# Optimization experiments

Hardware: AMD Instinct MI355X
Metric: run time of the kernel (lower is better)

Reference implementation:

```python
import jax, jax.numpy as jnp
import numpy as np

N_EXPERTS = 8
TOP_K = 2
D_MODEL = 1024
D_INNER = 4096
BATCH = 8
SEQ = 2048


def setup_inputs() -> dict:
    key = jax.random.key(0)
    k_x, k_g, k_e = jax.random.split(key, 3)
    sequences = jax.random.normal(k_x, (BATCH, SEQ, D_MODEL), dtype=jnp.float32)
    # gating Linear(d_model -> n_experts)
    gating_w = jax.random.normal(k_g, (N_EXPERTS, D_MODEL), dtype=jnp.float32) * (1.0 / np.sqrt(D_MODEL))
    gating_b = jnp.zeros((N_EXPERTS,), dtype=jnp.float32)
    # expert Linear(d_model -> d_inner), xavier_uniform
    xav = float(np.sqrt(6.0 / (D_MODEL + D_INNER)))
    expert_w = jax.random.uniform(k_e, (N_EXPERTS, D_INNER, D_MODEL), dtype=jnp.float32, minval=-xav, maxval=xav)
    expert_b = jnp.zeros((N_EXPERTS, D_INNER), dtype=jnp.float32)
    return {"sequences": sequences, "gating_w": gating_w, "gating_b": gating_b,
            "expert_w": expert_w, "expert_b": expert_b}


def reference(sequences, gating_w, gating_b, expert_w, expert_b):
    N, P, D = sequences.shape
    x = sequences.reshape(N * P, D)                                  # [T, D]
    gating_scores = jax.nn.softmax(x @ gating_w.T + gating_b, axis=-1)  # [T, E]
    _, top_k_indices = jax.lax.top_k(gating_scores, TOP_K)          # [T, K]
    # mask[t, e] = expert e is among token t's top-k (indices are distinct)
    mask = (top_k_indices[:, :, None] == jnp.arange(N_EXPERTS)[None, None, :]).any(axis=1)  # [T, E]
    maskf = mask.astype(x.dtype)
    out = jnp.zeros((N * P, D_INNER), dtype=x.dtype)
    for e in range(N_EXPERTS):  # small fixed expert count
        out = out + maskf[:, e:e + 1] * (x @ expert_w[e].T + expert_b[e])
    out = out / TOP_K
    # training-mode auxiliary: per-expert variance of gating scores (unbiased, like torch.var)
    gating_variances = jnp.var(gating_scores, axis=0, ddof=1)        # [E]
    return out.reshape(N, P, D_INNER), gating_variances
```

## Files before the change

### kernel.cpp

```cpp
#include <hip/hip_runtime.h>

#define T_TOKENS 16384
#define DM 1024
#define DI 4096
#define NE 8
#define PAIRS 64
#define CAP 16384

typedef float f32x4 __attribute__((ext_vector_type(4)));
typedef __bf16 bf16x8 __attribute__((ext_vector_type(8)));

__device__ inline unsigned short f2b(float f) {
  union { float f; unsigned u; } v; v.f = f;
  unsigned r = v.u + 0x7FFFu + ((v.u >> 16) & 1u);
  return (unsigned short)(r >> 16);
}

__global__ __launch_bounds__(256) void k_gating(
    const float* __restrict__ x, const float* __restrict__ gw, const float* __restrict__ gb,
    unsigned short* __restrict__ x16, float* __restrict__ scores,
    int* __restrict__ cnt, int* __restrict__ ptok)
{
  int wid  = (blockIdx.x * 256 + threadIdx.x) >> 6;
  int lane = threadIdx.x & 63;
  if (wid >= T_TOKENS) return;
  const float* xr = x + (size_t)wid * DM;

  double acc[NE];
  #pragma unroll
  for (int e = 0; e < NE; e++) acc[e] = 0.0;

  #pragma unroll
  for (int u = 0; u < 4; u++) {
    int off = u * 256 + lane * 4;
    float4 xv = *(const float4*)(xr + off);
    ushort4 pk; pk.x = f2b(xv.x); pk.y = f2b(xv.y); pk.z = f2b(xv.z); pk.w = f2b(xv.w);
    *(ushort4*)(x16 + (size_t)wid * DM + off) = pk;
    #pragma unroll
    for (int e = 0; e < NE; e++) {
      float4 wv = *(const float4*)(gw + e * DM + off);
      acc[e] += (double)xv.x * wv.x + (double)xv.y * wv.y
              + (double)xv.z * wv.z + (double)xv.w * wv.w;
    }
  }
  #pragma unroll
  for (int e = 0; e < NE; e++) {
    double v = acc[e];
    #pragma unroll
    for (int s = 32; s > 0; s >>= 1) v += __shfl_xor(v, s, 64);
    acc[e] = v + (double)gb[e];
  }
  if (lane == 0) {
    double m = acc[0];
    for (int e = 1; e < NE; e++) if (acc[e] > m) m = acc[e];
    double ex[NE], sum = 0.0;
    for (int e = 0; e < NE; e++) { ex[e] = exp(acc[e] - m); sum += ex[e]; }
    double inv = 1.0 / sum;
    for (int e = 0; e < NE; e++) scores[(size_t)wid * NE + e] = (float)(ex[e] * inv);
    int e1 = 0; double b1 = acc[0];
    for (int e = 1; e < NE; e++) if (acc[e] > b1) { b1 = acc[e]; e1 = e; }
    int e2 = -1; double b2 = -1e300;
    for (int e = 0; e < NE; e++) if (e != e1 && acc[e] > b2) { b2 = acc[e]; e2 = e; }
    int lo = e1 < e2 ? e1 : e2, hi = e1 < e2 ? e2 : e1;
    int p = lo * 8 + hi;
    int pos = atomicAdd(&cnt[p], 1);
    ptok[p * CAP + pos] = wid;
  }
}

__global__ __launch_bounds__(256) void k_wconv(const float* __restrict__ w, unsigned short* __restrict__ w16) {
  size_t i = ((size_t)blockIdx.x * 256 + threadIdx.x) * 8;
  float4 a = *(const float4*)(w + i);
  float4 b = *(const float4*)(w + i + 4);
  ushort4 pa, pb;
  pa.x = f2b(a.x); pa.y = f2b(a.y); pa.z = f2b(a.z); pa.w = f2b(a.w);
  pb.x = f2b(b.x); pb.y = f2b(b.y); pb.z = f2b(b.z); pb.w = f2b(b.w);
  *(ushort4*)(w16 + i) = pa;
  *(ushort4*)(w16 + i + 4) = pb;
}

__global__ void k_sched(const int* __restrict__ cnt, int* __restrict__ tiles, int* __restrict__ ntiles) {
  int p = threadIdx.x;
  int c = cnt[p];
  int nt = (c + 127) >> 7;
  int inc = nt;
  #pragma unroll
  for (int s = 1; s < 64; s <<= 1) {
    int v = __shfl_up(inc, s, 64);
    if (p >= s) inc += v;
  }
  int excl = inc - nt;
  for (int i = 0; i < nt; i++) { tiles[2 * (excl + i)] = p; tiles[2 * (excl + i) + 1] = i * 128; }
  if (p == 63) *ntiles = inc;
}

__global__ __launch_bounds__(256) void k_gemm(
    const unsigned short* __restrict__ x16, const unsigned short* __restrict__ w16,
    const float* __restrict__ eb, const int* __restrict__ cnt,
    const int* __restrict__ ptok, const int* __restrict__ tiles, const int* __restrict__ ntiles,
    float* __restrict__ out)
{
  __shared__ unsigned short As[128 * 64];
  __shared__ unsigned short Bs[2][128 * 64];

  int tileIdx = blockIdx.y;
  if (tileIdx >= *ntiles) return;
  int p    = tiles[2 * tileIdx];
  int row0 = tiles[2 * tileIdx + 1];
  int e1 = p >> 3, e2 = p & 7;
  int c  = cnt[p];
  int nTile = blockIdx.x;
  int tid  = threadIdx.x;
  int lane = tid & 63;
  int wid  = tid >> 6;
  int waveM = wid >> 1, waveN = wid & 1;

  int rlim = c - row0 - waveM * 64;

  int tok[4];
  #pragma unroll
  for (int i = 0; i < 4; i++) {
    int rg = row0 + (tid >> 3) + i * 32;
    if (rg > c - 1) rg = c - 1;
    tok[i] = ptok[p * CAP + rg];
  }

  f32x4 acc[4][4];
  #pragma unroll
  for (int i = 0; i < 4; i++)
    #pragma unroll
    for (int j = 0; j < 4; j++) acc[i][j] = {0.f, 0.f, 0.f, 0.f};

  const unsigned short* bb1 = w16 + ((size_t)e1 * DI + (size_t)nTile * 128) * DM;
  const unsigned short* bb2 = w16 + ((size_t)e2 * DI + (size_t)nTile * 128) * DM;

  for (int k0 = 0; k0 < DM; k0 += 64) {
    #pragma unroll
    for (int i = 0; i < 4; i++) {
      int r  = (tid >> 3) + i * 32;
      int cS = tid & 7;
      int kg = ((cS ^ (r & 7)) * 8);
      __builtin_amdgcn_global_load_lds(
          (const __attribute__((address_space(1))) void*)(x16 + (size_t)tok[i] * DM + k0 + kg),
          (__attribute__((address_space(3))) void*)(&As[r * 64 + cS * 8]), 16, 0, 0);
      __builtin_amdgcn_global_load_lds(
          (const __attribute__((address_space(1))) void*)(bb1 + (size_t)r * DM + k0 + kg),
          (__attribute__((address_space(3))) void*)(&Bs[0][r * 64 + cS * 8]), 16, 0, 0);
      __builtin_amdgcn_global_load_lds(
          (const __attribute__((address_space(1))) void*)(bb2 + (size_t)r * DM + k0 + kg),
          (__attribute__((address_space(3))) void*)(&Bs[1][r * 64 + cS * 8]), 16, 0, 0);
    }
    __syncthreads();
    #pragma unroll
    for (int kk = 0; kk < 2; kk++) {
      int q  = lane >> 4;
      int m  = lane & 15;
      int jg = kk * 4 + q;
      bf16x8 af[4], bf0[4], bf1[4];
      #pragma unroll
      for (int mi = 0; mi < 4; mi++) {
        if (mi * 16 < rlim) {
          int R = waveM * 64 + mi * 16 + m;
          af[mi] = *(const bf16x8*)&As[R * 64 + ((jg ^ (R & 7)) * 8)];
        }
      }
      #pragma unroll
      for (int ni = 0; ni < 4; ni++) {
        int R = waveN * 64 + ni * 16 + m;
        int o = R * 64 + ((jg ^ (R & 7)) * 8);
        bf0[ni] = *(const bf16x8*)&Bs[0][o];
        bf1[ni] = *(const bf16x8*)&Bs[1][o];
      }
      #pragma unroll
      for (int mi = 0; mi < 4; mi++) {
        if (mi * 16 < rlim) {
          #pragma unroll
          for (int ni = 0; ni < 4; ni++) {
            acc[mi][ni] = __builtin_amdgcn_mfma_f32_16x16x32_bf16(af[mi], bf0[ni], acc[mi][ni], 0, 0, 0);
            acc[mi][ni] = __builtin_amdgcn_mfma_f32_16x16x32_bf16(af[mi], bf1[ni], acc[mi][ni], 0, 0, 0);
          }
        }
      }
    }
    __syncthreads();
  }

  int colbase = nTile * 128 + waveN * 64;
  float bsum[4];
  #pragma unroll
  for (int ni = 0; ni < 4; ni++) {
    int col = colbase + ni * 16 + (lane & 15);
    bsum[ni] = 0.5f * (eb[e1 * DI + col] + eb[e2 * DI + col]);
  }
  #pragma unroll
  for (int mi = 0; mi < 4; mi++) {
    #pragma unroll
    for (int r2 = 0; r2 < 4; r2++) {
      int row = waveM * 64 + mi * 16 + (lane >> 4) * 4 + r2;
      int rg = row0 + row;
      if (rg < c) {
        int t = ptok[p * CAP + rg];
        float* orow = out + (size_t)t * DI + colbase;
        #pragma unroll
        for (int ni = 0; ni < 4; ni++)
          orow[ni * 16 + (lane & 15)] = 0.5f * acc[mi][ni][r2] + bsum[ni];
      }
    }
  }
}

__global__ __launch_bounds__(256) void k_var(const float* __restrict__ scores, float* __restrict__ vout) {
  int e = blockIdx.x, tid = threadIdx.x;
  double s = 0.0, s2 = 0.0;
  for (int t = tid; t < T_TOKENS; t += 256) {
    double v = (double)scores[(size_t)t * NE + e];
    s += v; s2 += v * v;
  }
  __shared__ double ls[256], ls2[256];
  ls[tid] = s; ls2[tid] = s2; __syncthreads();
  for (int st = 128; st > 0; st >>= 1) {
    if (tid < st) { ls[tid] += ls[tid + st]; ls2[tid] += ls2[tid + st]; }
    __syncthreads();
  }
  if (tid == 0) {
    double mean = ls[0] / (double)T_TOKENS;
    vout[e] = (float)((ls2[0] - ls[0] * mean) / (double)(T_TOKENS - 1));
  }
}

extern "C" void kernel_launch(void* const* d_in, const int* in_sizes, int n_in,
                              void* d_out, int out_size, void* d_ws, size_t ws_size,
                              hipStream_t stream)
{
  const float* x  = (const float*)d_in[0];
  const float* gw = (const float*)d_in[1];
  const float* gb = (const float*)d_in[2];
  const float* ew = (const float*)d_in[3];
  const float* eb = (const float*)d_in[4];
  float* out = (float*)d_out;

  char* ws = (char*)d_ws;
  unsigned short* x16 = (unsigned short*)ws;
  unsigned short* w16 = (unsigned short*)(ws + 33554432);
  float* scores       = (float*)(ws + 100663296);
  int*   ptok         = (int*)(ws + 101187584);
  int*   cnt          = (int*)(ws + 105381888);
  int*   ntiles       = (int*)(ws + 105382144);
  int*   tiles        = (int*)(ws + 105382160);

  hipMemsetAsync(cnt, 0, PAIRS * sizeof(int), stream);
  k_gating<<<dim3(4096), dim3(256), 0, stream>>>(x, gw, gb, x16, scores, cnt, ptok);
  k_wconv <<<dim3(16384), dim3(256), 0, stream>>>(ew, w16);
  k_sched <<<dim3(1), dim3(64), 0, stream>>>(cnt, tiles, ntiles);
  k_gemm  <<<dim3(32, 192), dim3(256), 0, stream>>>(x16, w16, eb, cnt, ptok, tiles, ntiles, out);
  k_var   <<<dim3(8), dim3(256), 0, stream>>>(scores, out + 67108864);
}
```

Baseline: 770.8 us.

## Double-buffer LDS tiles with K=32 stages to overlap loads with MFMA

Changes the GEMM main loop from single-buffered K=64 tiles with two barriers per step to double-buffered K=32 tiles. The next stage's global-to-LDS loads are issued before computing on the current buffer, leaving one barrier per step. LDS use stays the same, the swizzle is adapted to 32-wide rows, and launch bounds request 3 blocks per CU. The costs are twice as many iterations and barriers, and more register pressure from the occupancy hint.

```diff
diff --git a/kernel.cpp b/kernel.cpp
--- a/kernel.cpp
+++ b/kernel.cpp
@@ -94,14 +94,14 @@
   if (p == 63) *ntiles = inc;
 }
 
-__global__ __launch_bounds__(256) void k_gemm(
+__global__ __launch_bounds__(256, 3) void k_gemm(
     const unsigned short* __restrict__ x16, const unsigned short* __restrict__ w16,
     const float* __restrict__ eb, const int* __restrict__ cnt,
     const int* __restrict__ ptok, const int* __restrict__ tiles, const int* __restrict__ ntiles,
     float* __restrict__ out)
 {
-  __shared__ unsigned short As[128 * 64];
-  __shared__ unsigned short Bs[2][128 * 64];
+  __shared__ unsigned short As[2][128 * 32];
+  __shared__ unsigned short Bs[2][2][128 * 32];
 
   int tileIdx = blockIdx.y;
   if (tileIdx >= *ntiles) return;
@@ -117,10 +117,10 @@
 
   int rlim = c - row0 - waveM * 64;
 
-  int tok[4];
-  #pragma unroll
-  for (int i = 0; i < 4; i++) {
-    int rg = row0 + (tid >> 3) + i * 32;
+  int tok[2];
+  #pragma unroll
+  for (int i = 0; i < 2; i++) {
+    int rg = row0 + (tid >> 2) + i * 64;
     if (rg > c - 1) rg = c - 1;
     tok[i] = ptok[p * CAP + rg];
   }
@@ -134,56 +134,66 @@
   const unsigned short* bb1 = w16 + ((size_t)e1 * DI + (size_t)nTile * 128) * DM;
   const unsigned short* bb2 = w16 + ((size_t)e2 * DI + (size_t)nTile * 128) * DM;
 
-  for (int k0 = 0; k0 < DM; k0 += 64) {
-    #pragma unroll
-    for (int i = 0; i < 4; i++) {
-      int r  = (tid >> 3) + i * 32;
-      int cS = tid & 7;
-      int kg = ((cS ^ (r & 7)) * 8);
-      __builtin_amdgcn_global_load_lds(
-          (const __attribute__((address_space(1))) void*)(x16 + (size_t)tok[i] * DM + k0 + kg),
-          (__attribute__((address_space(3))) void*)(&As[r * 64 + cS * 8]), 16, 0, 0);
-      __builtin_amdgcn_global_load_lds(
-          (const __attribute__((address_space(1))) void*)(bb1 + (size_t)r * DM + k0 + kg),
-          (__attribute__((address_space(3))) void*)(&Bs[0][r * 64 + cS * 8]), 16, 0, 0);
-      __builtin_amdgcn_global_load_lds(
-          (const __attribute__((address_space(1))) void*)(bb2 + (size_t)r * DM + k0 + kg),
-          (__attribute__((address_space(3))) void*)(&Bs[1][r * 64 + cS * 8]), 16, 0, 0);
-    }
-    __syncthreads();
-    #pragma unroll
-    for (int kk = 0; kk < 2; kk++) {
-      int q  = lane >> 4;
-      int m  = lane & 15;
-      int jg = kk * 4 + q;
-      bf16x8 af[4], bf0[4], bf1[4];
-      #pragma unroll
-      for (int mi = 0; mi < 4; mi++) {
-        if (mi * 16 < rlim) {
-          int R = waveM * 64 + mi * 16 + m;
-          af[mi] = *(const bf16x8*)&As[R * 64 + ((jg ^ (R & 7)) * 8)];
+#define STAGE(buf, k0s)                                                                           \
+  {                                                                                               \
+    _Pragma("unroll")                                                                             \
+    for (int i = 0; i < 2; i++) {                                                                 \
+      int r  = (tid >> 2) + i * 64;                                                               \
+      int cS = tid & 3;                                                                           \
+      int kg = ((cS ^ ((r >> 1) & 3)) * 8);               \
+      __builtin_amdgcn_global_load_lds(                                                           \
+          (const __attribute__((address_space(1))) void*)(x16 + (size_t)tok[i] * DM + (k0s) + kg),\
+          (__attribute__((address_space(3))) void*)(&As[buf][r * 32 + cS * 8]), 16, 0, 0);        \
+      __builtin_amdgcn_global_load_lds(                                                           \
+          (const __attribute__((address_space(1))) void*)(bb1 + (size_t)r * DM + (k0s) + kg),     \
+          (__attribute__((address_space(3))) void*)(&Bs[buf][0][r * 32 + cS * 8]), 16, 0, 0);     \
+      __builtin_amdgcn_global_load_lds(                                                           \
+          (const __attribute__((address_space(1))) void*)(bb2 + (size_t)r * DM + (k0s) + kg),     \
+          (__attribute__((address_space(3))) void*)(&Bs[buf][1][r * 32 + cS * 8]), 16, 0, 0);     \
+    }                                                                                             \
+  }
+
+  int cur = 0;
+  STAGE(0, 0);
+
+  #pragma unroll 2
+  for (int k0 = 0; k0 < DM; k0 += 32) {
+    asm volatile("s_waitcnt vmcnt(0)" ::: "memory");
+    __builtin_amdgcn_s_barrier();
+    __builtin_amdgcn_sched_barrier(0);
+
+    if (k0 + 32 < DM) { STAGE(cur ^ 1, k0 + 32); }
+
+    int q = lane >> 4;
+    int m = lane & 15;
+    bf16x8 af[4], bf0[4], bf1[4];
+    #pragma unroll
+    for (int mi = 0; mi < 4; mi++) {
+      if (mi * 16 < rlim) {
+        int R = waveM * 64 + mi * 16 + m;
+        af[mi] = *(const bf16x8*)&As[cur][R * 32 + ((q ^ ((R >> 1) & 3)) * 8)];
+      }
+    }
+    #pragma unroll
+    for (int ni = 0; ni < 4; ni++) {
+      int R = waveN * 64 + ni * 16 + m;
+      int o = R * 32 + ((q ^ ((R >> 1) & 3)) * 8);
+      bf0[ni] = *(const bf16x8*)&Bs[cur][0][o];
+      bf1[ni] = *(const bf16x8*)&Bs[cur][1][o];
+    }
+    #pragma unroll
+    for (int mi = 0; mi < 4; mi++) {
+      if (mi * 16 < rlim) {
+        #pragma unroll
+        for (int ni = 0; ni < 4; ni++) {
+          acc[mi][ni] = __builtin_amdgcn_mfma_f32_16x16x32_bf16(af[mi], bf0[ni], acc[mi][ni], 0, 0, 0);
+          acc[mi][ni] = __builtin_amdgcn_mfma_f32_16x16x32_bf16(af[mi], bf1[ni], acc[mi][ni], 0, 0, 0);
         }
       }
-      #pragma unroll
-      for (int ni = 0; ni < 4; ni++) {
-        int R = waveN * 64 + ni * 16 + m;
-        int o = R * 64 + ((jg ^ (R & 7)) * 8);
-        bf0[ni] = *(const bf16x8*)&Bs[0][o];
-        bf1[ni] = *(const bf16x8*)&Bs[1][o];
-      }
-      #pragma unroll
-      for (int mi = 0; mi < 4; mi++) {
-        if (mi * 16 < rlim) {
-          #pragma unroll
-          for (int ni = 0; ni < 4; ni++) {
-            acc[mi][ni] = __builtin_amdgcn_mfma_f32_16x16x32_bf16(af[mi], bf0[ni], acc[mi][ni], 0, 0, 0);
-            acc[mi][ni] = __builtin_amdgcn_mfma_f32_16x16x32_bf16(af[mi], bf1[ni], acc[mi][ni], 0, 0, 0);
-          }
-        }
-      }
-    }
-    __syncthreads();
-  }
+    }
+    cur ^= 1;
+  }
+#undef STAGE
 
   int colbase = nTile * 128 + waveN * 64;
   float bsum[4];
```

Result: slower. 790.8 us (+2.6%).

## Precombine expert-pair weights so each token tile runs a single GEMM

Applied to the files above, without the earlier changes.

Adds a kernel that builds averaged bf16 weight matrices for all 28 expert pairs, (W_lo+W_hi)/2. The grouped GEMM can then multiply each token tile by one pair matrix instead of accumulating two expert GEMMs, which halves the MFMA work and the B-operand traffic. The cost is writing 28 bf16 weight matrices (about 235 MB) per call instead of 8. Rounding the average to bf16 also changes numerics slightly. A fallback keeps the old dual-expert path when the workspace is too small, and the new GEMM uses a single B buffer with a launch-bounds occupancy hint.

```diff
diff --git a/kernel.cpp b/kernel.cpp
--- a/kernel.cpp
+++ b/kernel.cpp
@@ -5,6 +5,7 @@
 #define DI 4096
 #define NE 8
 #define PAIRS 64
+#define NPAIRC 28
 #define CAP 16384
 
 typedef float f32x4 __attribute__((ext_vector_type(4)));
@@ -79,6 +80,27 @@
   *(ushort4*)(w16 + i + 4) = pb;
 }
 
+__global__ __launch_bounds__(256) void k_wpair(const float* __restrict__ w, unsigned short* __restrict__ wp) {
+  size_t i = ((size_t)blockIdx.x * 256 + threadIdx.x) * 4;
+  float4 v[NE];
+  #pragma unroll
+  for (int e = 0; e < NE; e++) v[e] = *(const float4*)(w + (size_t)e * (DI * (size_t)DM) + i);
+  int idx = 0;
+  #pragma unroll
+  for (int lo = 0; lo < NE; lo++) {
+    #pragma unroll
+    for (int hi = lo + 1; hi < NE; hi++) {
+      ushort4 pk;
+      pk.x = f2b(0.5f * (v[lo].x + v[hi].x));
+      pk.y = f2b(0.5f * (v[lo].y + v[hi].y));
+      pk.z = f2b(0.5f * (v[lo].z + v[hi].z));
+      pk.w = f2b(0.5f * (v[lo].w + v[hi].w));
+      *(ushort4*)(wp + (size_t)idx * (DI * (size_t)DM) + i) = pk;
+      idx++;
+    }
+  }
+}
+
 __global__ void k_sched(const int* __restrict__ cnt, int* __restrict__ tiles, int* __restrict__ ntiles) {
   int p = threadIdx.x;
   int c = cnt[p];
@@ -94,7 +116,115 @@
   if (p == 63) *ntiles = inc;
 }
 
-__global__ __launch_bounds__(256) void k_gemm(
+__global__ __launch_bounds__(256, 5) void k_gemm_pair(
+    const unsigned short* __restrict__ x16, const unsigned short* __restrict__ wp,
+    const float* __restrict__ eb, const int* __restrict__ cnt,
+    const int* __restrict__ ptok, const int* __restrict__ tiles, const int* __restrict__ ntiles,
+    float* __restrict__ out)
+{
+  __shared__ unsigned short As[128 * 64];
+  __shared__ unsigned short Bs[128 * 64];
+
+  int tileIdx = blockIdx.y;
+  if (tileIdx >= *ntiles) return;
+  int p    = tiles[2 * tileIdx];
+  int row0 = tiles[2 * tileIdx + 1];
+  int e1 = p >> 3, e2 = p & 7;
+  int pidx = e1 * 7 - ((e1 * (e1 - 1)) >> 1) + (e2 - e1 - 1);
+  int c  = cnt[p];
+  int nTile = blockIdx.x;
+  int tid  = threadIdx.x;
+  int lane = tid & 63;
+  int wid  = tid >> 6;
+  int waveM = wid >> 1, waveN = wid & 1;
+
+  int rlim = c - row0 - waveM * 64;
+
+  int tok[4];
+  #pragma unroll
+  for (int i = 0; i < 4; i++) {
+    int rg = row0 + (tid >> 3) + i * 32;
+    if (rg > c - 1) rg = c - 1;
+    tok[i] = ptok[p * CAP + rg];
+  }
+
+  f32x4 acc[4][4];
+  #pragma unroll
+  for (int i = 0; i < 4; i++)
+    #pragma unroll
+    for (int j = 0; j < 4; j++) acc[i][j] = {0.f, 0.f, 0.f, 0.f};
+
+  const unsigned short* bb = wp + ((size_t)pidx * DI + (size_t)nTile * 128) * DM;
+
+  for (int k0 = 0; k0 < DM; k0 += 64) {
+    #pragma unroll
+    for (int i = 0; i < 4; i++) {
+      int r  = (tid >> 3) + i * 32;
+      int cS = tid & 7;
+      int kg = ((cS ^ (r & 7)) * 8);
+      __builtin_amdgcn_global_load_lds(
+          (const __attribute__((address_space(1))) void*)(x16 + (size_t)tok[i] * DM + k0 + kg),
+          (__attribute__((address_space(3))) void*)(&As[r * 64 + cS * 8]), 16, 0, 0);
+      __builtin_amdgcn_global_load_lds(
+          (const __attribute__((address_space(1))) void*)(bb + (size_t)r * DM + k0 + kg),
+          (__attribute__((address_space(3))) void*)(&Bs[r * 64 + cS * 8]), 16, 0, 0);
+    }
+    __syncthreads();
+    #pragma unroll
+    for (int kk = 0; kk < 2; kk++) {
+      int q  = lane >> 4;
+      int m  = lane & 15;
+      int jg = kk * 4 + q;
+      bf16x8 af[4], bf[4];
+      #pragma unroll
+      for (int mi = 0; mi < 4; mi++) {
+        if (mi * 16 < rlim) {
+          int R = waveM * 64 + mi * 16 + m;
+          af[mi] = *(const bf16x8*)&As[R * 64 + ((jg ^ (R & 7)) * 8)];
+        }
+      }
+      #pragma unroll
+      for (int ni = 0; ni < 4; ni++) {
+        int R = waveN * 64 + ni * 16 + m;
+        bf[ni] = *(const bf16x8*)&Bs[R * 64 + ((jg ^ (R & 7)) * 8)];
+      }
+      #pragma unroll
+      for (int mi = 0; mi < 4; mi++) {
+        if (mi * 16 < rlim) {
+          #pragma unroll
+          for (int ni = 0; ni < 4; ni++)
+            acc[mi][ni] = __builtin_amdgcn_mfma_f32_16x16x32_bf16(af[mi], bf[ni], acc[mi][ni], 0, 0, 0);
+        }
+      }
+    }
+    __syncthreads();
+  }
+
+  int colbase = nTile * 128 + waveN * 64;
+  float bsum[4];
+  #pragma unroll
+  for (int ni = 0; ni < 4; ni++) {
+    int col = colbase + ni * 16 + (lane & 15);
+    bsum[ni] = 0.5f * (eb[e1 * DI + col] + eb[e2 * DI + col]);
+  }
+  #pragma unroll
+  for (int mi = 0; mi < 4; mi++) {
+    #pragma unroll
+    for (int r2 = 0; r2 < 4; r2++) {
+      int row = waveM * 64 + mi * 16 + (lane >> 4) * 4 + r2;
+      int rg = row0 + row;
+      if (rg < c) {
+        int t = ptok[p * CAP + rg];
+        float* orow = out + (size_t)t * DI + colbase;
+        #pragma unroll
+        for (int ni = 0; ni < 4; ni++)
+          orow[ni * 16 + (lane & 15)] = acc[mi][ni][r2] + bsum[ni];
+      }
+    }
+  }
+}
+
+__global__ __launch_bounds__(256) void k_gemm_dual(
     const unsigned short* __restrict__ x16, const unsigned short* __restrict__ w16,
     const float* __restrict__ eb, const int* __restrict__ cnt,
     const int* __restrict__ ptok, const int* __restrict__ tiles, const int* __restrict__ ntiles,
@@ -114,7 +244,6 @@
   int lane = tid & 63;
   int wid  = tid >> 6;
   int waveM = wid >> 1, waveN = wid & 1;
-
   int rlim = c - row0 - waveM * 64;
 
   int tok[4];
@@ -238,20 +367,45 @@
   const float* ew = (const float*)d_in[3];
   const float* eb = (const float*)d_in[4];
   float* out = (float*)d_out;
-
   char* ws = (char*)d_ws;
-  unsigned short* x16 = (unsigned short*)ws;
-  unsigned short* w16 = (unsigned short*)(ws + 33554432);
-  float* scores       = (float*)(ws + 100663296);
-  int*   ptok         = (int*)(ws + 101187584);
-  int*   cnt          = (int*)(ws + 105381888);
-  int*   ntiles       = (int*)(ws + 105382144);
-  int*   tiles        = (int*)(ws + 105382160);
-
-  hipMemsetAsync(cnt, 0, PAIRS * sizeof(int), stream);
-  k_gating<<<dim3(4096), dim3(256), 0, stream>>>(x, gw, gb, x16, scores, cnt, ptok);
-  k_wconv <<<dim3(16384), dim3(256), 0, stream>>>(ew, w16);
-  k_sched <<<dim3(1), dim3(64), 0, stream>>>(cnt, tiles, ntiles);
-  k_gemm  <<<dim3(32, 192), dim3(256), 0, stream>>>(x16, w16, eb, cnt, ptok, tiles, ntiles, out);
-  k_var   <<<dim3(8), dim3(256), 0, stream>>>(scores, out + 67108864);
-}
+
+  const size_t OFF_WPAIR  = 33554432ull;
+  const size_t OFF_SCORES = OFF_WPAIR + (size_t)NPAIRC * DI * DM * 2;
+  const size_t OFF_PTOK   = OFF_SCORES + 524288ull;
+  const size_t OFF_CNT    = OFF_PTOK + 4194304ull;
+  const size_t OFF_NT     = OFF_CNT + 256ull;
+  const size_t OFF_TILES  = OFF_NT + 16ull;
+  const size_t NEED_PAIR  = OFF_TILES + 1536ull;
+
+  if (ws_size >= NEED_PAIR) {
+    unsigned short* x16 = (unsigned short*)ws;
+    unsigned short* wp  = (unsigned short*)(ws + OFF_WPAIR);
+    float* scores       = (float*)(ws + OFF_SCORES);
+    int*   ptok         = (int*)(ws + OFF_PTOK);
+    int*   cnt          = (int*)(ws + OFF_CNT);
+    int*   ntiles       = (int*)(ws + OFF_NT);
+    int*   tiles        = (int*)(ws + OFF_TILES);
+
+    hipMemsetAsync(cnt, 0, PAIRS * sizeof(int), stream);
+    k_gating<<<dim3(4096), dim3(256), 0, stream>>>(x, gw, gb, x16, scores, cnt, ptok);
+    k_wpair <<<dim3(4096), dim3(256), 0, stream>>>(ew, wp);
+    k_sched <<<dim3(1), dim3(64), 0, stream>>>(cnt, tiles, ntiles);
+    k_gemm_pair<<<dim3(32, 192), dim3(256), 0, stream>>>(x16, wp, eb, cnt, ptok, tiles, ntiles, out);
+    k_var   <<<dim3(8), dim3(256), 0, stream>>>(scores, out + 67108864);
+  } else {
+    unsigned short* x16 = (unsigned short*)ws;
+    unsigned short* w16 = (unsigned short*)(ws + 33554432);
+    float* scores       = (float*)(ws + 100663296);
+    int*   ptok         = (int*)(ws + 101187584);
+    int*   cnt          = (int*)(ws + 105381888);
+    int*   ntiles       = (int*)(ws + 105382144);
+    int*   tiles        = (int*)(ws + 105382160);
+
+    hipMemsetAsync(cnt, 0, PAIRS * sizeof(int), stream);
+    k_gating<<<dim3(4096), dim3(256), 0, stream>>>(x, gw, gb, x16, scores, cnt, ptok);
+    k_wconv <<<dim3(16384), dim3(256), 0, stream>>>(ew, w16);
+    k_sched <<<dim3(1), dim3(64), 0, stream>>>(cnt, tiles, ntiles);
+    k_gemm_dual<<<dim3(32, 192), dim3(256), 0, stream>>>(x16, w16, eb, cnt, ptok, tiles, ntiles, out);
+    k_var   <<<dim3(8), dim3(256), 0, stream>>>(scores, out + 67108864);
+  }
+}
```

Result: slower. 1.490 ms (+93.3%).
